# Optimization experiments

Hardware: AMD Instinct MI355X
Metric: run time of the kernel (lower is better)

Reference implementation:

```python
import jax, jax.numpy as jnp
import numpy as np

B, C, T = 64, 128, 500
N_RES, N_CLASSES = 2048, 10
DECAY_RES, DECAY_CLF = 0.9, 0.9
V_TH_RES, V_TH_CLF = 1.0, 1.0


def setup_inputs() -> dict:
    key = jax.random.key(0)
    k1, k2, k3, k4 = jax.random.split(key, 4)
    x = jax.random.normal(k1, (B, C, T), dtype=jnp.float32)
    # learned / fixed parameters sized per init_kwargs
    W_in = jax.random.normal(k2, (N_RES, C), dtype=jnp.float32) * (1.0 / np.sqrt(C))
    W_res = jax.random.normal(k3, (N_RES, N_RES), dtype=jnp.float32) * (1.0 / np.sqrt(N_RES))
    W_clf = jax.random.normal(k4, (N_CLASSES, N_RES), dtype=jnp.float32) * (1.0 / np.sqrt(N_RES))
    return {"x": x, "W_in": W_in, "W_res": W_res, "W_clf": W_clf}


def reference(x, W_in, W_res, W_clf):
    """x: (B, C, T). Returns (spike_counts (B, n_classes), reservoir_spikes_accum (B, n_reservoir)).
    LIF reservoir + single-voter LIF readout, no STDP updates (use_stdp=False path)."""
    Bb = x.shape[0]
    dtype = x.dtype

    def step(carry, x_t):  # x_t: (B, C)
        v_r, s_prev, v_c = carry
        # reservoir LIF: leak + feedforward input + recurrent spike input
        I = x_t @ W_in.T + s_prev @ W_res.T          # (B, N_RES)
        v_r = DECAY_RES * v_r + I
        s = (v_r >= V_TH_RES).astype(dtype)          # spike
        v_r = v_r * (1.0 - s)                        # reset fired neurons
        # classifier (STDPLayer forward, plasticity disabled)
        v_c = DECAY_CLF * v_c + s @ W_clf.T          # (B, N_CLASSES)
        c = (v_c >= V_TH_CLF).astype(dtype)
        v_c = v_c * (1.0 - c)
        return (v_r, s, v_c), (c, s)

    init = (jnp.zeros((Bb, N_RES), dtype),
            jnp.zeros((Bb, N_RES), dtype),
            jnp.zeros((Bb, N_CLASSES), dtype))
    xs = jnp.moveaxis(x, 2, 0)                       # (T, B, C)
    _, (clf_spikes, res_spikes) = jax.lax.scan(step, init, xs)
    spike_counts = clf_spikes.sum(axis=0)            # (B, N_CLASSES)
    reservoir_spikes_accum = res_spikes.sum(axis=0)  # (B, N_RES)
    return spike_counts, reservoir_spikes_accum
```

## Files before the change

kernel.cpp:

```cpp
#include <hip/hip_runtime.h>
#include <cstdint>
#include <cstddef>

#define B_    64
#define C_    128
#define T_    500
#define NRES  2048
#define NCLS  10

#define NWG   256
#define SL    8
#define NT    1024
#define WROW  520
#define WPIT  (4 * WROW)
#define XSP   132



#define WS_MASK0   0
#define WS_MASK1   16384
#define WS_FLAG    32768
#define WS_ARR     49152
#define WS_WORDS   13312
#define NFLAG      16
#define CHKWG      (NWG - 1)

typedef float v2f __attribute__((ext_vector_type(2)));

struct SMem {
  float    WtT2[SL][WPIT];
  float    WinT2[SL][C_];
  float    xs[B_][XSP];
  unsigned maskb[2][B_][65];
  double   clfred2[2][NCLS];
};

__global__ void zero_ws_kernel(unsigned* __restrict__ p, int n) {
  int i = blockIdx.x * blockDim.x + threadIdx.x;
  if (i < n) p[i] = 0u;
}

#define ACC2(ACC, WB, M0, M1, JB) do {                                        \
  const unsigned _lo = (unsigned)(((int)((M0) << (31 - (JB)))) >> 31) & (WB); \
  const unsigned _hi = (unsigned)(((int)((M1) << (31 - (JB)))) >> 31) & (WB); \
  v2f _m; _m.x = __uint_as_float(_lo); _m.y = __uint_as_float(_hi);           \
  (ACC) = (ACC) + _m;                                                         \
} while (0)

#define BT_STEP(X, D, MLO) do {                                            \
  const unsigned _y = (unsigned)__shfl_xor((int)(X), (D), 64);             \
  (X) = (b & (D)) ? (((X) & ~(MLO)) | ((_y >> (D)) & (MLO)))               \
                  : (((X) & (MLO)) | ((_y << (D)) & ~(MLO)));              \
} while (0)

#define BT_ALL(X) do {                 \
  BT_STEP(X, 16, 0x0000FFFFu);         \
  BT_STEP(X,  8, 0x00FF00FFu);         \
  BT_STEP(X,  4, 0x0F0F0F0Fu);         \
  BT_STEP(X,  2, 0x33333333u);         \
  BT_STEP(X,  1, 0x55555555u);         \
} while (0)

__device__ __forceinline__ float g1_compute(const float* __restrict__ winrow,
                                            const float* __restrict__ xrow) {
  float g1 = 0.f;
  const float4* __restrict__ winp = (const float4*)winrow;
  const float4* __restrict__ xrp  = (const float4*)xrow;
  #pragma unroll 8
  for (int cq = 0; cq < 32; ++cq) {
    const float4 wv = winp[cq];
    const float4 xq = xrp[cq];
    g1 = fmaf(xq.x, wv.x, g1);
    g1 = fmaf(xq.y, wv.y, g1);
    g1 = fmaf(xq.z, wv.z, g1);
    g1 = fmaf(xq.w, wv.w, g1);
  }
  return g1;
}

__global__ void __launch_bounds__(NT, 4)
reservoir_kernel(const float* __restrict__ x, const float* __restrict__ Win,
                 const float* __restrict__ Wres, const float* __restrict__ Wclf,
                 float* __restrict__ out, unsigned char* __restrict__ ws) {
  __shared__ SMem sm;
  const int w   = blockIdx.x;
  const int tid = threadIdx.x;
  const int b   = tid & 63;
  const int wid = tid >> 6;
  const int il  = wid & 7;
  const int h   = wid >> 3;
  const int blk = b & 3;
  const int g   = b >> 2;
  const int bat0 = h * 32 + g * 2;
  const int bat1 = bat0 + 1;
  const int iu  = __builtin_amdgcn_readfirstlane(w * SL + il);
  const int bat = h * 32 + (b & 31);

  unsigned* gm0  = (unsigned*)(ws + WS_MASK0);
  unsigned* gm1  = (unsigned*)(ws + WS_MASK1);
  unsigned* flgb = (unsigned*)(ws + WS_FLAG);
  unsigned* arr  = (unsigned*)(ws + WS_ARR);
  unsigned* myflag = flgb + (w & (NFLAG - 1)) * 256;

  {
    const int j0 = tid * 16;
    #pragma unroll
    for (int r4 = 0; r4 < 4; ++r4) {
      const int j   = j0 + r4 * 4;
      const int il2 = j >> 11;
      const int pos = j & 2047;
      const int bk  = pos >> 9;
      const int s   = pos & 511;
      const float4 v4 = *(const float4*)(Wres + (size_t)(w * SL + il2) * NRES + pos);
      *(float4*)(&sm.WtT2[il2][bk * WROW + s]) = v4;
    }
  }
  {
    const int il2 = tid >> 7, c = tid & 127;
    sm.WinT2[il2][c] = Win[(size_t)(w * SL + il2) * C_ + c];
  }

  float v = 0.f;
  int   cntr = 0;
  double vc = 0.0;
  int   cntc = 0;

  float xv[8];
  {
    const int p0 = tid * 8;
    float tmp[8];
    #pragma unroll
    for (int r = 0; r < 8; ++r) tmp[r] = x[(size_t)(p0 + r) * T_ + 0];
    float4 fa, fb;
    fa.x = tmp[0]; fa.y = tmp[1]; fa.z = tmp[2]; fa.w = tmp[3];
    fb.x = tmp[4]; fb.y = tmp[5]; fb.z = tmp[6]; fb.w = tmp[7];
    const int row = p0 >> 7, col = p0 & 127;
    *(float4*)(&sm.xs[row][col])     = fa;
    *(float4*)(&sm.xs[row][col + 4]) = fb;
    #pragma unroll
    for (int r = 0; r < 8; ++r) xv[r] = x[(size_t)(p0 + r) * T_ + 1];
  }
  __syncthreads();

  float g1cur = 0.f;
  if (b < 32) g1cur = g1_compute(&sm.WinT2[il][0], &sm.xs[bat][0]);

  for (int t = 0; t < T_; ++t) {
    unsigned* gprev = (t & 1) ? gm0 : gm1;
    unsigned* gcur  = (t & 1) ? gm1 : gm0;
    unsigned (* __restrict__ mk)[65] = sm.maskb[t & 1];

    {
      const int i32 = b & 31, hh = b >> 5;
      #pragma unroll
      for (int kk = 0; kk < 4; ++kk) {
        const int k = (wid << 2) | kk;
        unsigned xw = __hip_atomic_load(gprev + (k * 32 + i32) * 2 + hh,
                                        __ATOMIC_RELAXED, __HIP_MEMORY_SCOPE_AGENT);
        BT_ALL(xw);
        mk[b][k] = xw;
      }
    }
    __syncthreads();

    if (t + 1 < T_) {
      const int p0 = tid * 8;
      float4 fa, fb;
      fa.x = xv[0]; fa.y = xv[1]; fa.z = xv[2]; fa.w = xv[3];
      fb.x = xv[4]; fb.y = xv[5]; fb.z = xv[6]; fb.w = xv[7];
      const int row = p0 >> 7, col = p0 & 127;
      *(float4*)(&sm.xs[row][col])     = fa;
      *(float4*)(&sm.xs[row][col + 4]) = fb;
      if (t + 2 < T_) {
        #pragma unroll
        for (int r = 0; r < 8; ++r) xv[r] = x[(size_t)(p0 + r) * T_ + (t + 2)];
      }
    }

    v2f acc; acc.x = 0.f; acc.y = 0.f;
    {
      const float*    wbase = &sm.WtT2[il][blk * WROW];
      const unsigned* mr0   = &mk[bat0][blk * 16];
      const unsigned* mr1   = &mk[bat1][blk * 16];
      #pragma unroll 4
      for (int wq = 0; wq < 16; ++wq) {
        const unsigned m0 = mr0[wq];
        const unsigned m1 = mr1[wq];
        const float4* q = (const float4*)(wbase + wq * 32);
        #pragma unroll
        for (int jq = 0; jq < 8; ++jq) {
          const float4 w4 = q[jq];
          const int jb = jq * 4;
          ACC2(acc, __float_as_uint(w4.x), m0, m1, jb + 0);
          ACC2(acc, __float_as_uint(w4.y), m0, m1, jb + 1);
          ACC2(acc, __float_as_uint(w4.z), m0, m1, jb + 2);
          ACC2(acc, __float_as_uint(w4.w), m0, m1, jb + 3);
        }
      }
    }
    const float aP = acc.x, aQ = acc.y;

    const float p1 = __shfl_xor(aP, 1), q1 = __shfl_xor(aQ, 1);
    const float p2 = __shfl_xor(aP, 2), q2 = __shfl_xor(aQ, 2);
    const float p3 = __shfl_xor(aP, 3), q3 = __shfl_xor(aQ, 3);
    const float g2u0 = __fadd_rn(__fadd_rn(__fadd_rn(aP, p1), p2), p3);
    const float g2u1 = __fadd_rn(__fadd_rn(__fadd_rn(aQ, q1), q2), q3);

    {
      const int src = (b >> 1) * 4;
      const float r0 = __shfl(g2u0, src, 64);
      const float r1 = __shfl(g2u1, src, 64);
      const float g2m = (b & 1) ? r1 : r0;
      const float I = __fadd_rn(g1cur, g2m);
      v = __fadd_rn(__fmul_rn(0.9f, v), I);
      bool s = (b < 32) && (v >= 1.0f);
      if (s) { v = 0.f; cntr++; }
      unsigned long long bal = __ballot(s);
      if (b == 0)
        __hip_atomic_store(gcur + iu * 2 + h, (unsigned)bal,
                           __ATOMIC_RELAXED, __HIP_MEMORY_SCOPE_AGENT);
    }
    __syncthreads();

    if (tid == 0)
      __hip_atomic_store(arr + w * 4, (unsigned)(t + 1),
                         __ATOMIC_RELEASE, __HIP_MEMORY_SCOPE_AGENT);


    if (t + 1 < T_ && b < 32)
      g1cur = g1_compute(&sm.WinT2[il][0], &sm.xs[bat][0]);

    if (w == CHKWG && wid == 0) {
      const unsigned tgt = (unsigned)(t + 1);
      for (;;) {
        unsigned a0 = __hip_atomic_load(arr + (b +   0) * 4, __ATOMIC_RELAXED,
                                        __HIP_MEMORY_SCOPE_AGENT);
        unsigned a1 = __hip_atomic_load(arr + (b +  64) * 4, __ATOMIC_RELAXED,
                                        __HIP_MEMORY_SCOPE_AGENT);
        unsigned a2 = __hip_atomic_load(arr + (b + 128) * 4, __ATOMIC_RELAXED,
                                        __HIP_MEMORY_SCOPE_AGENT);
        unsigned a3 = __hip_atomic_load(arr + (b + 192) * 4, __ATOMIC_RELAXED,
                                        __HIP_MEMORY_SCOPE_AGENT);
        bool ok = (a0 >= tgt) & (a1 >= tgt) & (a2 >= tgt) & (a3 >= tgt);
        if (__all(ok)) break;
        __builtin_amdgcn_s_sleep(1);
      }
      if (b < NFLAG)
        __hip_atomic_store(flgb + b * 256, (unsigned)(t + 1),
                           __ATOMIC_RELEASE, __HIP_MEMORY_SCOPE_AGENT);
    }

    if (w < B_) {
      if (wid < NCLS) {
        double pc = 0.0;
        if (t > 0) {
          const float* __restrict__ wc = Wclf + (size_t)wid * NRES + b;
          #pragma unroll 4
          for (int q = 0; q < 32; ++q) {
            const unsigned mw = mk[w][(b >> 5) + 2 * q];
            const float wv = wc[q * 64];
            const unsigned keep =
                (unsigned)(((int)(mw << (31 - (b & 31)))) >> 31);
            pc += (double)__uint_as_float(keep & __float_as_uint(wv));
          }
        }
        #pragma unroll
        for (int off = 1; off < 64; off <<= 1)
          pc += __shfl_xor(pc, off, 64);
        if (b == 0) sm.clfred2[t & 1][wid] = pc;
      }
      if (tid < NCLS && t >= 2) {
        vc = 0.9 * vc + sm.clfred2[(t + 1) & 1][tid];
        if (vc >= 1.0) { vc = 0.0; cntc++; }
      }
    }

    while (__hip_atomic_load(myflag, __ATOMIC_RELAXED,
                             __HIP_MEMORY_SCOPE_AGENT) < (unsigned)(t + 1))
      __builtin_amdgcn_s_sleep(1);
  }

  __syncthreads();
  if (w < B_ && tid < NCLS) {
    vc = 0.9 * vc + sm.clfred2[1][tid];
    if (vc >= 1.0) { vc = 0.0; cntc++; }
  }
  {
    const int i32 = b & 31, hh = b >> 5;
    #pragma unroll
    for (int kk = 0; kk < 4; ++kk) {
      const int k = (wid << 2) | kk;
      unsigned xw = __hip_atomic_load(gm1 + (k * 32 + i32) * 2 + hh,
                                      __ATOMIC_RELAXED, __HIP_MEMORY_SCOPE_AGENT);
      BT_ALL(xw);
      sm.maskb[0][b][k] = xw;
    }
  }
  __syncthreads();
  if (w < B_ && wid < NCLS) {
    double pc = 0.0;
    {
      const float* __restrict__ wc = Wclf + (size_t)wid * NRES + b;
      #pragma unroll 4
      for (int q = 0; q < 32; ++q) {
        const unsigned mw = sm.maskb[0][w][(b >> 5) + 2 * q];
        const float wv = wc[q * 64];
        const unsigned keep =
            (unsigned)(((int)(mw << (31 - (b & 31)))) >> 31);
        pc += (double)__uint_as_float(keep & __float_as_uint(wv));
      }
    }
    #pragma unroll
    for (int off = 1; off < 64; off <<= 1)
      pc += __shfl_xor(pc, off, 64);
    if (b == 0) sm.clfred2[0][wid] = pc;
  }
  __syncthreads();
  if (w < B_ && tid < NCLS) {
    vc = 0.9 * vc + sm.clfred2[0][tid];
    if (vc >= 1.0) cntc++;
    out[w * NCLS + tid] = (float)cntc;
  }
  if (b < 32)
    out[B_ * NCLS + (size_t)bat * NRES + w * SL + il] = (float)cntr;
}

extern "C" void kernel_launch(void* const* d_in, const int* in_sizes, int n_in,
                              void* d_out, int out_size, void* d_ws, size_t ws_size,
                              hipStream_t stream) {
  const float* x    = (const float*)d_in[0];
  const float* Win  = (const float*)d_in[1];
  const float* Wres = (const float*)d_in[2];
  const float* Wclf = (const float*)d_in[3];
  float* out = (float*)d_out;
  unsigned char* ws = (unsigned char*)d_ws;

  hipLaunchKernelGGL(zero_ws_kernel, dim3((WS_WORDS + 255) / 256), dim3(256), 0, stream,
                     (unsigned*)ws, WS_WORDS);
  hipLaunchKernelGGL(reservoir_kernel, dim3(NWG), dim3(NT), 0, stream,
                     x, Win, Wres, Wclf, out, ws);
}
```

Baseline: 13.65 ms.

## Split reservoir neuron reduction across wave halves via LDS partial sums

Reassigns work so each wave pair splits the 2048-column recurrent dot product by column block instead of by batch half. One wave writes partial sums to a new LDS buffer, and the other finishes the reduction, applies the LIF update for all 64 batches, and publishes a 64-bit spike ballot. This replaces the cross-lane shuffle reduction and removes idle lanes in the neuron update, at the cost of an extra __syncthreads per timestep. Classifier work moves onto the first-half waves with a loop over classes.

Result: no change. 13.74 ms (+0.6%).

```diff
diff --git a/kernel.cpp b/kernel.cpp
--- a/kernel.cpp
+++ b/kernel.cpp
@@ -14,7 +14,6 @@
 #define WROW  520
 #define WPIT  (4 * WROW)
 #define XSP   132
-
 
 
 #define WS_MASK0   0
@@ -32,6 +31,7 @@
   float    WinT2[SL][C_];
   float    xs[B_][XSP];
   unsigned maskb[2][B_][65];
+  float    s01buf[SL][68];
   double   clfred2[2][NCLS];
 };
 
@@ -88,13 +88,11 @@
   const int b   = tid & 63;
   const int wid = tid >> 6;
   const int il  = wid & 7;
-  const int h   = wid >> 3;
-  const int blk = b & 3;
-  const int g   = b >> 2;
-  const int bat0 = h * 32 + g * 2;
-  const int bat1 = bat0 + 1;
+  const int p   = wid >> 3;
+  const int blk = 2 * p + (b & 1);
+  const int bat0 = b & ~1;
+  const int bat1 = b | 1;
   const int iu  = __builtin_amdgcn_readfirstlane(w * SL + il);
-  const int bat = h * 32 + (b & 31);
 
   unsigned* gm0  = (unsigned*)(ws + WS_MASK0);
   unsigned* gm1  = (unsigned*)(ws + WS_MASK1);
@@ -143,7 +141,7 @@
   __syncthreads();
 
   float g1cur = 0.f;
-  if (b < 32) g1cur = g1_compute(&sm.WinT2[il][0], &sm.xs[bat][0]);
+  if (p) g1cur = g1_compute(&sm.WinT2[il][0], &sm.xs[b][0]);
 
   for (int t = 0; t < T_; ++t) {
     unsigned* gprev = (t & 1) ? gm0 : gm1;
@@ -198,26 +196,30 @@
         }
       }
     }
-    const float aP = acc.x, aQ = acc.y;
-
-    const float p1 = __shfl_xor(aP, 1), q1 = __shfl_xor(aQ, 1);
-    const float p2 = __shfl_xor(aP, 2), q2 = __shfl_xor(aQ, 2);
-    const float p3 = __shfl_xor(aP, 3), q3 = __shfl_xor(aQ, 3);
-    const float g2u0 = __fadd_rn(__fadd_rn(__fadd_rn(aP, p1), p2), p3);
-    const float g2u1 = __fadd_rn(__fadd_rn(__fadd_rn(aQ, q1), q2), q3);
-
-    {
-      const int src = (b >> 1) * 4;
-      const float r0 = __shfl(g2u0, src, 64);
-      const float r1 = __shfl(g2u1, src, 64);
-      const float g2m = (b & 1) ? r1 : r0;
-      const float I = __fadd_rn(g1cur, g2m);
+
+    if (!p) {
+      const float shx = __shfl_xor(acc.x, 1);
+      const float shy = __shfl_xor(acc.y, 1);
+      const float s01x = __fadd_rn(acc.x, shx);
+      const float s01y = __fadd_rn(acc.y, shy);
+      sm.s01buf[il][b] = (b & 1) ? s01y : s01x;
+    }
+    __syncthreads();
+
+    if (p) {
+      const float shx = __shfl_xor(acc.x, 1);
+      const float shy = __shfl_xor(acc.y, 1);
+      const float a2 = (b & 1) ? shy : acc.x;
+      const float a3 = (b & 1) ? acc.y : shx;
+      const float s01 = sm.s01buf[il][b];
+      const float g2 = __fadd_rn(__fadd_rn(s01, a2), a3);
+      const float I  = __fadd_rn(g1cur, g2);
       v = __fadd_rn(__fmul_rn(0.9f, v), I);
-      bool s = (b < 32) && (v >= 1.0f);
+      const bool s = (v >= 1.0f);
       if (s) { v = 0.f; cntr++; }
-      unsigned long long bal = __ballot(s);
+      const unsigned long long bal = __ballot(s);
       if (b == 0)
-        __hip_atomic_store(gcur + iu * 2 + h, (unsigned)bal,
+        __hip_atomic_store((unsigned long long*)gcur + iu, bal,
                            __ATOMIC_RELAXED, __HIP_MEMORY_SCOPE_AGENT);
     }
     __syncthreads();
@@ -227,8 +229,8 @@
                          __ATOMIC_RELEASE, __HIP_MEMORY_SCOPE_AGENT);
 
 
-    if (t + 1 < T_ && b < 32)
-      g1cur = g1_compute(&sm.WinT2[il][0], &sm.xs[bat][0]);
+    if (p && t + 1 < T_)
+      g1cur = g1_compute(&sm.WinT2[il][0], &sm.xs[b][0]);
 
     if (w == CHKWG && wid == 0) {
       const unsigned tgt = (unsigned)(t + 1);
@@ -237,11 +239,11 @@
                                         __HIP_MEMORY_SCOPE_AGENT);
         unsigned a1 = __hip_atomic_load(arr + (b +  64) * 4, __ATOMIC_RELAXED,
                                         __HIP_MEMORY_SCOPE_AGENT);
-        unsigned a2 = __hip_atomic_load(arr + (b + 128) * 4, __ATOMIC_RELAXED,
-                                        __HIP_MEMORY_SCOPE_AGENT);
-        unsigned a3 = __hip_atomic_load(arr + (b + 192) * 4, __ATOMIC_RELAXED,
-                                        __HIP_MEMORY_SCOPE_AGENT);
-        bool ok = (a0 >= tgt) & (a1 >= tgt) & (a2 >= tgt) & (a3 >= tgt);
+        unsigned a2c = __hip_atomic_load(arr + (b + 128) * 4, __ATOMIC_RELAXED,
+                                         __HIP_MEMORY_SCOPE_AGENT);
+        unsigned a3c = __hip_atomic_load(arr + (b + 192) * 4, __ATOMIC_RELAXED,
+                                         __HIP_MEMORY_SCOPE_AGENT);
+        bool ok = (a0 >= tgt) & (a1 >= tgt) & (a2c >= tgt) & (a3c >= tgt);
         if (__all(ok)) break;
         __builtin_amdgcn_s_sleep(1);
       }
@@ -251,23 +253,25 @@
     }
 
     if (w < B_) {
-      if (wid < NCLS) {
-        double pc = 0.0;
-        if (t > 0) {
-          const float* __restrict__ wc = Wclf + (size_t)wid * NRES + b;
-          #pragma unroll 4
-          for (int q = 0; q < 32; ++q) {
-            const unsigned mw = mk[w][(b >> 5) + 2 * q];
-            const float wv = wc[q * 64];
-            const unsigned keep =
-                (unsigned)(((int)(mw << (31 - (b & 31)))) >> 31);
-            pc += (double)__uint_as_float(keep & __float_as_uint(wv));
+      if (!p) {
+        for (int c = wid; c < NCLS; c += 8) {
+          double pc = 0.0;
+          if (t > 0) {
+            const float* __restrict__ wc = Wclf + (size_t)c * NRES + b;
+            #pragma unroll 4
+            for (int q = 0; q < 32; ++q) {
+              const unsigned mw = mk[w][(b >> 5) + 2 * q];
+              const float wv = wc[q * 64];
+              const unsigned keep =
+                  (unsigned)(((int)(mw << (31 - (b & 31)))) >> 31);
+              pc += (double)__uint_as_float(keep & __float_as_uint(wv));
+            }
           }
+          #pragma unroll
+          for (int off = 1; off < 64; off <<= 1)
+            pc += __shfl_xor(pc, off, 64);
+          if (b == 0) sm.clfred2[t & 1][c] = pc;
         }
-        #pragma unroll
-        for (int off = 1; off < 64; off <<= 1)
-          pc += __shfl_xor(pc, off, 64);
-        if (b == 0) sm.clfred2[t & 1][wid] = pc;
       }
       if (tid < NCLS && t >= 2) {
         vc = 0.9 * vc + sm.clfred2[(t + 1) & 1][tid];
@@ -321,8 +325,8 @@
     if (vc >= 1.0) cntc++;
     out[w * NCLS + tid] = (float)cntc;
   }
-  if (b < 32)
-    out[B_ * NCLS + (size_t)bat * NRES + w * SL + il] = (float)cntr;
+  if (p)
+    out[B_ * NCLS + (size_t)b * NRES + w * SL + il] = (float)cntr;
 }
 
 extern "C" void kernel_launch(void* const* d_in, const int* in_sizes, int n_in,
```
